# Kernel tuning notes

Measured on AMD Instinct MI355X. Metric: run time of the kernel, lower is better.

The kernel has to match this reference:

```python
import jax, jax.numpy as jnp
import numpy as np

SCALE = 1.0 / np.sqrt(2.0).astype(np.float32)  # 1/sqrt(head_dim=2)


def setup_inputs() -> dict:
    key = jax.random.key(0)
    k1, k2 = jax.random.split(key)
    shape = (1, 2048, 8, 2)  # (batch, seq_len, heads, spinor_dim=2)
    return {
        "spinors_real": jax.random.normal(k1, shape, dtype=jnp.float32),
        "spinors_imag": jax.random.normal(k2, shape, dtype=jnp.float32),
    }


def reference(spinors_real, spinors_imag):
    # assemble complex spinors (batch, seq, heads, 2)
    spinors = jax.lax.complex(spinors_real, spinors_imag)
    # L2 norm over the spinor dim (real-valued magnitude norm, as torch.norm on cfloat)
    nrm = jnp.sqrt(jnp.sum(spinors_real * spinors_real + spinors_imag * spinors_imag,
                           axis=-1, keepdims=True))
    normed = spinors / nrm
    # Hermitian inner product logits: (b, i, j, h)
    logits = jnp.einsum('bihd,bjhd->bijh', jnp.conj(normed), normed)
    # softmax over key axis j of the real part, scaled
    attn = jax.nn.softmax(logits.real * SCALE, axis=2)
    # combine original (unnormalized) spinors
    out = jnp.einsum('bijh,bjhd->bihd', attn.astype(spinors.dtype), spinors)
    return out
```

## Files before the change

### kernel.cpp

```cpp
#include <hip/hip_runtime.h>


#define S 2048
#define H 8
#define QR 4
#define NW 8
#define TPB (NW * 64)

typedef float vf2 __attribute__((ext_vector_type(2)));

__device__ inline float fast_exp2(float x) {
#if __has_builtin(__builtin_amdgcn_exp2f)
    return __builtin_amdgcn_exp2f(x);
#else
    return exp2f(x);
#endif
}

__global__ __launch_bounds__(TPB, 4) void su2_attn_fused(
        const float* __restrict__ re, const float* __restrict__ im,
        float2* __restrict__ outr, float2* __restrict__ outi) {
    __shared__ float4 vt[S];
    __shared__ float  nt[S];

    const int h    = blockIdx.y;
    const int lane = threadIdx.x & 63;
    const int wave = threadIdx.x >> 6;
    const int i_base = (blockIdx.x * NW + wave) * QR;

    const float2* __restrict__ re2 = (const float2*)re;
    const float2* __restrict__ im2 = (const float2*)im;
#pragma unroll
    for (int k = 0; k < S / TPB; ++k) {
        int j = k * TPB + threadIdx.x;
        float2 r = re2[j * H + h];
        float2 m = im2[j * H + h];
        float ss = r.x * r.x + m.x * m.x + r.y * r.y + m.y * m.y;
        vt[j] = make_float4(r.x, m.x, r.y, m.y);
        nt[j] = rsqrtf(ss);
    }
    __syncthreads();

    const float c = 0.70710678118654752440f * 1.44269504088896340736f;
    vf2 qc0[QR], qc1[QR];
#pragma unroll
    for (int r = 0; r < QR; ++r) {
        float4 v = vt[i_base + r];
        float  s = nt[i_base + r] * c;
        vf2 q0 = {v.x * s, v.y * s};
        vf2 q1 = {v.z * s, v.w * s};
        qc0[r] = q0;
        qc1[r] = q1;
    }

    float l[QR];
    vf2 a0[QR], a1[QR];
#pragma unroll
    for (int r = 0; r < QR; ++r) {
        l[r]  = 0.f;
        a0[r] = (vf2){0.f, 0.f};
        a1[r] = (vf2){0.f, 0.f};
    }

#pragma unroll 4
    for (int jj = 0; jj < S / 64; ++jj) {
        int j = jj * 64 + lane;
        float4 v   = vt[j];
        float  inv = nt[j];
        vf2 v0 = {v.x, v.y};
        vf2 v1 = {v.z, v.w};
#pragma unroll
        for (int r = 0; r < QR; ++r) {
            vf2 d2 = __builtin_elementwise_fma(qc1[r], v1, qc0[r] * v0);
            float p = fast_exp2((d2.x + d2.y) * inv);
            l[r] += p;
            vf2 pp = {p, p};
            a0[r] = __builtin_elementwise_fma(pp, v0, a0[r]);
            a1[r] = __builtin_elementwise_fma(pp, v1, a1[r]);
        }
    }

#pragma unroll
    for (int r = 0; r < QR; ++r) {
#pragma unroll
        for (int m = 32; m >= 1; m >>= 1) {
            l[r]    += __shfl_xor(l[r], m, 64);
            a0[r].x += __shfl_xor(a0[r].x, m, 64);
            a0[r].y += __shfl_xor(a0[r].y, m, 64);
            a1[r].x += __shfl_xor(a1[r].x, m, 64);
            a1[r].y += __shfl_xor(a1[r].y, m, 64);
        }
    }

    if (lane == 0) {
#pragma unroll
        for (int r = 0; r < QR; ++r) {
            float invl = 1.0f / l[r];
            int i = i_base + r;
            outr[i * H + h] = make_float2(a0[r].x * invl, a1[r].x * invl);
            outi[i * H + h] = make_float2(a0[r].y * invl, a1[r].y * invl);
        }
    }
}

extern "C" void kernel_launch(void* const* d_in, const int* in_sizes, int n_in,
                              void* d_out, int out_size, void* d_ws, size_t ws_size,
                              hipStream_t stream) {
    const float* re = (const float*)d_in[0];
    const float* im = (const float*)d_in[1];
    float2* outr = (float2*)d_out;
    float2* outi = outr + S * H;
    (void)d_ws; (void)ws_size;

    su2_attn_fused<<<dim3(S / (NW * QR), H), dim3(TPB), 0, stream>>>(re, im, outr, outi);
}
```

Measured before the change: 68.89 us.

## Overlap key staging with compute by processing own-wave chunk before barrier

Each wave now loads its query spinors straight from global memory instead of through shared memory. It stages its own 256 keys into LDS and processes those keys immediately, before the block barrier. After the barrier it walks the remaining 28 chunks in a rotated order starting after its own. This aims to hide the barrier wait and the global-load latency behind useful exp/FMA work. It also rewrites the shuffle reduction to use vector adds, and the summation order changes slightly.

```diff
diff --git a/kernel.cpp b/kernel.cpp
--- a/kernel.cpp
+++ b/kernel.cpp
@@ -30,27 +30,30 @@
 
     const float2* __restrict__ re2 = (const float2*)re;
     const float2* __restrict__ im2 = (const float2*)im;
+
+    const float c = 0.70710678118654752440f * 1.44269504088896340736f;
+    vf2 qc0[QR], qc1[QR];
 #pragma unroll
-    for (int k = 0; k < S / TPB; ++k) {
-        int j = k * TPB + threadIdx.x;
+    for (int r = 0; r < QR; ++r) {
+        int i = i_base + r;
+        float2 qr = re2[i * H + h];
+        float2 qi = im2[i * H + h];
+        float ss = qr.x * qr.x + qi.x * qi.x + qr.y * qr.y + qi.y * qi.y;
+        float s  = rsqrtf(ss) * c;
+        vf2 q0 = {qr.x * s, qi.x * s};
+        vf2 q1 = {qr.y * s, qi.y * s};
+        qc0[r] = q0;
+        qc1[r] = q1;
+    }
+
+#pragma unroll
+    for (int it = 0; it < 4; ++it) {
+        int j = (wave * 4 + it) * 64 + lane;
         float2 r = re2[j * H + h];
         float2 m = im2[j * H + h];
         float ss = r.x * r.x + m.x * m.x + r.y * r.y + m.y * m.y;
         vt[j] = make_float4(r.x, m.x, r.y, m.y);
         nt[j] = rsqrtf(ss);
-    }
-    __syncthreads();
-
-    const float c = 0.70710678118654752440f * 1.44269504088896340736f;
-    vf2 qc0[QR], qc1[QR];
-#pragma unroll
-    for (int r = 0; r < QR; ++r) {
-        float4 v = vt[i_base + r];
-        float  s = nt[i_base + r] * c;
-        vf2 q0 = {v.x * s, v.y * s};
-        vf2 q1 = {v.z * s, v.w * s};
-        qc0[r] = q0;
-        qc1[r] = q1;
     }
 
     float l[QR];
@@ -62,9 +65,29 @@
         a1[r] = (vf2){0.f, 0.f};
     }
 
+#pragma unroll
+    for (int t = 0; t < 4; ++t) {
+        int j = (wave * 4 + t) * 64 + lane;
+        float4 v   = vt[j];
+        float  inv = nt[j];
+        vf2 v0 = {v.x, v.y};
+        vf2 v1 = {v.z, v.w};
+#pragma unroll
+        for (int r = 0; r < QR; ++r) {
+            vf2 d2 = __builtin_elementwise_fma(qc1[r], v1, qc0[r] * v0);
+            float p = fast_exp2((d2.x + d2.y) * inv);
+            l[r] += p;
+            vf2 pp = {p, p};
+            a0[r] = __builtin_elementwise_fma(pp, v0, a0[r]);
+            a1[r] = __builtin_elementwise_fma(pp, v1, a1[r]);
+        }
+    }
+    __syncthreads();
+
 #pragma unroll 4
-    for (int jj = 0; jj < S / 64; ++jj) {
-        int j = jj * 64 + lane;
+    for (int t = 4; t < 32; ++t) {
+        int jju = (wave * 4 + t) & 31;
+        int j = jju * 64 + lane;
         float4 v   = vt[j];
         float  inv = nt[j];
         vf2 v0 = {v.x, v.y};
@@ -84,11 +107,14 @@
     for (int r = 0; r < QR; ++r) {
 #pragma unroll
         for (int m = 32; m >= 1; m >>= 1) {
-            l[r]    += __shfl_xor(l[r], m, 64);
-            a0[r].x += __shfl_xor(a0[r].x, m, 64);
-            a0[r].y += __shfl_xor(a0[r].y, m, 64);
-            a1[r].x += __shfl_xor(a1[r].x, m, 64);
-            a1[r].y += __shfl_xor(a1[r].y, m, 64);
+            l[r] += __shfl_xor(l[r], m, 64);
+            vf2 t0, t1;
+            t0.x = __shfl_xor(a0[r].x, m, 64);
+            t0.y = __shfl_xor(a0[r].y, m, 64);
+            t1.x = __shfl_xor(a1[r].x, m, 64);
+            t1.y = __shfl_xor(a1[r].y, m, 64);
+            a0[r] += t0;
+            a1[r] += t1;
         }
     }
 
```

After: 71.82 us. +4.3%, slower.
